# Performance work log

Measured on AMD Instinct MI355X. Metric: run time of the kernel, lower is better.

The kernel has to match this reference:

```python
import jax, jax.numpy as jnp
import numpy as np


def table_operator(A, B):
    # A, B: (size, batch). Returns (16, size, batch) of soft logic-gate outputs.
    AB = A * B
    A_or_B = A + B - AB
    A_xor_B = A + B - 2.0 * AB
    return jnp.stack([
        jnp.zeros_like(A),          # 0: FALSE
        AB,                         # 1: A AND B
        A - AB,                     # 2: A AND NOT B
        A,                          # 3: A
        B - AB,                     # 4: NOT A AND B
        B,                          # 5: B
        A_xor_B,                    # 6: A XOR B
        A_or_B,                     # 7: A OR B
        1.0 - A_or_B,               # 8: NOR
        1.0 - A_xor_B,              # 9: XNOR
        1.0 - B,                    # 10: NOT B
        1.0 - B + AB,               # 11: B -> A
        1.0 - A,                    # 12: NOT A
        1.0 - A + AB,               # 13: A -> B
        1.0 - AB,                   # 14: NAND
        jnp.ones_like(A),           # 15: TRUE
    ], axis=0)


def setup_inputs() -> dict:
    key = jax.random.key(0)
    k1, k2, k3, k4 = jax.random.split(key, 4)
    prev_size, size, batch = 1024, 1024, 16384
    return {
        "prev_layer_output": jax.random.uniform(k1, (prev_size, batch), jnp.float32),
        "input_A_weights": jax.random.normal(k2, (size, prev_size), jnp.float32),
        "input_B_weights": jax.random.normal(k3, (size, prev_size), jnp.float32),
        "table_weights": jax.random.normal(k4, (16, size), jnp.float32),
    }


def reference(prev_layer_output, input_A_weights, input_B_weights, table_weights):
    # Inference path (torch.is_grad_enabled() == False, drop_out_rate == 0):
    # plain softmaxes, no multiplier shift, no dropout. GradFactor is identity in fwd.
    pA = jax.nn.softmax(input_A_weights, axis=1)   # (size, prev_size)
    pB = jax.nn.softmax(input_B_weights, axis=1)
    pT = jax.nn.softmax(table_weights, axis=0)     # (16, size)
    a = pA @ prev_layer_output                     # (size, batch)
    b = pB @ prev_layer_output                     # (size, batch)
    gates = table_operator(a, b)                   # (16, size, batch)
    return jnp.sum(gates * pT[:, :, None], axis=0)  # (size, batch)
```

## Files before the change

kernel.cpp:

```cpp
#include <hip/hip_runtime.h>
#include <hip/hip_bf16.h>


typedef __attribute__((ext_vector_type(8))) short bf16x8;
typedef __attribute__((ext_vector_type(4))) float f32x4;

__device__ __forceinline__ void gload_lds16(const void* g, void* l) {
    __builtin_amdgcn_global_load_lds(
        (const __attribute__((address_space(1))) void*)g,
        (__attribute__((address_space(3))) void*)l, 16, 0, 0);
}

__global__ __launch_bounds__(256) void softmax_rows_bf16(
    const float* __restrict__ WA, const float* __restrict__ WB,
    __hip_bfloat16* __restrict__ PA, __hip_bfloat16* __restrict__ PB,
    int rows, int cols)
{
    const int b = blockIdx.x;
    const float* W;
    __hip_bfloat16* P;
    if (b < rows) { W = WA + (size_t)b * cols;          P = PA + (size_t)b * cols; }
    else          { W = WB + (size_t)(b - rows) * cols; P = PB + (size_t)(b - rows) * cols; }

    const int t = threadIdx.x;
    const int wave = t >> 6, lane = t & 63;

    float4 v = *(const float4*)&W[t * 4];
    float mx = fmaxf(fmaxf(v.x, v.y), fmaxf(v.z, v.w));
    #pragma unroll
    for (int off = 32; off; off >>= 1) mx = fmaxf(mx, __shfl_xor(mx, off));

    __shared__ float redmax[4];
    __shared__ float redsum[4];
    if (lane == 0) redmax[wave] = mx;
    __syncthreads();
    mx = fmaxf(fmaxf(redmax[0], redmax[1]), fmaxf(redmax[2], redmax[3]));

    float e0 = __expf(v.x - mx), e1 = __expf(v.y - mx);
    float e2 = __expf(v.z - mx), e3 = __expf(v.w - mx);
    float s = e0 + e1 + e2 + e3;
    #pragma unroll
    for (int off = 32; off; off >>= 1) s += __shfl_xor(s, off);
    if (lane == 0) redsum[wave] = s;
    __syncthreads();
    s = redsum[0] + redsum[1] + redsum[2] + redsum[3];

    const float inv = 1.0f / s;
    __align__(8) __hip_bfloat16 o[4];
    o[0] = __float2bfloat16(e0 * inv);
    o[1] = __float2bfloat16(e1 * inv);
    o[2] = __float2bfloat16(e2 * inv);
    o[3] = __float2bfloat16(e3 * inv);
    *(uint2*)&P[t * 4] = *(const uint2*)o;
}

__global__ void table_coef(const float* __restrict__ TW, float4* __restrict__ coef, int size)
{
    const int s = blockIdx.x * blockDim.x + threadIdx.x;
    if (s >= size) return;
    float p[16];
    float mx = -1e30f;
    #pragma unroll
    for (int g = 0; g < 16; ++g) { p[g] = TW[g * size + s]; mx = fmaxf(mx, p[g]); }
    float sum = 0.f;
    #pragma unroll
    for (int g = 0; g < 16; ++g) { p[g] = __expf(p[g] - mx); sum += p[g]; }
    const float inv = 1.0f / sum;
    #pragma unroll
    for (int g = 0; g < 16; ++g) p[g] *= inv;

    float w0  = p[8] + p[9] + p[10] + p[11] + p[12] + p[13] + p[14] + p[15];
    float wA  = p[2] + p[3] + p[6] + p[7] - p[8] - p[9] - p[12] - p[13];
    float wB  = p[4] + p[5] + p[6] + p[7] - p[8] - p[9] - p[10] - p[11];
    float wAB = p[1] - p[2] - p[4] - 2.f * p[6] - p[7]
              + p[8] + 2.f * p[9] + p[11] + p[13] - p[14];
    coef[s] = make_float4(w0, wA, wB, wAB);
}

__global__ __launch_bounds__(256) void transpose_bf16(
    const float* __restrict__ prev, __hip_bfloat16* __restrict__ prevT,
    int K, int N)
{
    __shared__ float ls[64][65];
    const int k0 = blockIdx.y * 64, n0 = blockIdx.x * 64;
    const int t = threadIdx.x;

    {
        const int kr = t >> 4, nc = (t & 15) * 4;
        #pragma unroll
        for (int i = 0; i < 4; ++i) {
            const int k = i * 16 + kr;
            float4 v = *(const float4*)&prev[(size_t)(k0 + k) * N + n0 + nc];
            ls[k][nc + 0] = v.x; ls[k][nc + 1] = v.y;
            ls[k][nc + 2] = v.z; ls[k][nc + 3] = v.w;
        }
    }
    __syncthreads();
    {
        const int n = t >> 2, kc = (t & 3) * 16;
        __align__(16) __hip_bfloat16 tmp[16];
        #pragma unroll
        for (int j = 0; j < 16; ++j) tmp[j] = __float2bfloat16(ls[kc + j][n]);
        __hip_bfloat16* dst = &prevT[(size_t)(n0 + n) * K + k0 + kc];
        *(uint4*)(dst + 0) = *(const uint4*)&tmp[0];
        *(uint4*)(dst + 8) = *(const uint4*)&tmp[8];
    }
}

constexpr int Kd = 1024;
constexpr int Nd = 16384;

__global__ __launch_bounds__(512, 2) void dual_gemm8(
    const __hip_bfloat16* __restrict__ pA,
    const __hip_bfloat16* __restrict__ pB,
    const __hip_bfloat16* __restrict__ prevT,
    const float4* __restrict__ coef,
    float* __restrict__ out)
{
    __shared__ __align__(16) char smem[131072];

    const int t_ = threadIdx.x;
    const int wave = t_ >> 6, lane = t_ & 63;
    const int wr = wave >> 2, wc = wave & 3;
    const int m0 = blockIdx.y * 128;
    const int n0 = blockIdx.x * 256;

    const int fr  = lane & 15;
    const int kg  = lane >> 4;
    const int fsw = fr & 7;
    const int c0 = (kg ^ fsw) * 16;
    const int c1 = ((4 + kg) ^ fsw) * 16;
    const int aoffs = (wr * 128 + fr) * 128;
    const int boffs = 32768 + (wc * 64 + fr) * 128;

    const int sr  = lane >> 3;
    const int swz = ((lane & 7) ^ sr) * 8;
    const int r0  = wave * 16 + sr;
    const __hip_bfloat16* gA0 = pA    + (size_t)(m0 + r0) * Kd + swz;
    const __hip_bfloat16* gA1 = pB    + (size_t)(m0 + r0) * Kd + swz;
    const __hip_bfloat16* gB0 = prevT + (size_t)(n0 + r0) * Kd + swz;
    const __hip_bfloat16* gB1 = prevT + (size_t)(n0 + 128 + r0) * Kd + swz;

    f32x4 acc[8][4] = {};
    bf16x8 a[8], b[8];

#define STG(GP, BB, HOFF, KT) {                                             \
    char* lb = smem + (BB) + (HOFF) + wave * 2048;                          \
    gload_lds16((GP) + (KT), lb);                                           \
    gload_lds16((GP) + (KT) + 8 * Kd, lb + 1024); }

#define RD_ALO(BB) _Pragma("unroll") for (int i = 0; i < 4; ++i) {          \
    a[i*2]   = *(const bf16x8*)(smem + (BB) + aoffs + i * 2048 + c0);       \
    a[i*2+1] = *(const bf16x8*)(smem + (BB) + aoffs + i * 2048 + c1); }
#define RD_AHI(BB) _Pragma("unroll") for (int i = 0; i < 4; ++i) {          \
    a[i*2]   = *(const bf16x8*)(smem + (BB) + aoffs + 8192 + i * 2048 + c0);\
    a[i*2+1] = *(const bf16x8*)(smem + (BB) + aoffs + 8192 + i * 2048 + c1); }
#define RD_BLO(BB) _Pragma("unroll") for (int j = 0; j < 2; ++j) {          \
    b[j*2]   = *(const bf16x8*)(smem + (BB) + boffs + j * 2048 + c0);       \
    b[j*2+1] = *(const bf16x8*)(smem + (BB) + boffs + j * 2048 + c1); }
#define RD_BHI(BB) _Pragma("unroll") for (int j = 0; j < 2; ++j) {          \
    b[4+j*2]   = *(const bf16x8*)(smem + (BB) + boffs + 4096 + j * 2048 + c0); \
    b[4+j*2+1] = *(const bf16x8*)(smem + (BB) + boffs + 4096 + j * 2048 + c1); }

#define BAR __builtin_amdgcn_s_barrier()
#define VMW(S) asm volatile("s_waitcnt " S ::: "memory")

#define MM(I0, J0, BB0)                                                     \
    asm volatile("s_waitcnt lgkmcnt(0)" ::: "memory");                      \
    __builtin_amdgcn_sched_barrier(0);                                      \
    __builtin_amdgcn_s_setprio(1);                                          \
    _Pragma("unroll") for (int i = 0; i < 4; ++i)                           \
    _Pragma("unroll") for (int j = 0; j < 2; ++j)                           \
    _Pragma("unroll") for (int ks = 0; ks < 2; ++ks)                        \
        acc[(I0)+i][(J0)+j] = __builtin_amdgcn_mfma_f32_16x16x32_bf16(      \
            a[i*2+ks], b[(BB0)+j*2+ks], acc[(I0)+i][(J0)+j], 0, 0, 0);      \
    __builtin_amdgcn_s_setprio(0);

#define TILE(T, CURB, NXTB, SA, SB, VM1) {                                  \
    RD_ALO(CURB) RD_BLO(CURB)                                               \
    if (SA) STG(gA0, NXTB, 0, ((T)+1)*64)                                   \
    asm volatile("s_waitcnt lgkmcnt(8)" ::: "memory");                      \
    VMW(VM1); BAR;                                                          \
    MM(0, 0, 0) BAR;                                                        \
    RD_BHI(CURB)                                                            \
    if (SA) STG(gA1, NXTB, 16384, ((T)+1)*64)                               \
    VMW("vmcnt(6)"); BAR;                                                   \
    MM(0, 2, 4) BAR;                                                        \
    RD_AHI(CURB)                                                            \
    if (SB) STG(gB0, CURB, 32768, ((T)+2)*64)                               \
    VMW("vmcnt(6)"); BAR;                                                   \
    MM(4, 2, 4) BAR;                                                        \
    if (SB) STG(gB1, CURB, 49152, ((T)+2)*64)                               \
    VMW("vmcnt(6)"); BAR;                                                   \
    MM(4, 0, 0) BAR;                                                        \
}

    STG(gB0, 0, 32768, 0)
    STG(gB1, 0, 49152, 0)
    STG(gA0, 0, 0,     0)
    STG(gA1, 0, 16384, 0)
    STG(gB0, 65536, 32768, 64)
    STG(gB1, 65536, 49152, 64)
    VMW("vmcnt(4)");
    BAR;

    for (int t = 0; t < 14; t += 2) {
        TILE(t,     0,     65536, 1, 1, "vmcnt(6)")
        TILE(t + 1, 65536, 0,     1, 1, "vmcnt(6)")
    }
    TILE(14, 0,     65536, 1, 0, "vmcnt(6)")
    TILE(15, 65536, 0,     0, 0, "vmcnt(0)")

#undef TILE
#undef MM
#undef STG
#undef RD_ALO
#undef RD_AHI
#undef RD_BLO
#undef RD_BHI
#undef BAR
#undef VMW

    __syncthreads();
    if (wr == 1) {
        #pragma unroll
        for (int i = 0; i < 8; ++i) {
            #pragma unroll
            for (int j = 0; j < 4; ++j) {
                const int off = ((((wc * 8 + i) * 4 + j) * 64) + lane) * 16;
                *(f32x4*)(smem + off) = acc[i][j];
            }
        }
    }
    __syncthreads();
    if (wr == 0) {
        const int hi = lane >> 4;
        #pragma unroll
        for (int i = 0; i < 8; ++i) {
            float4 cc[4];
            #pragma unroll
            for (int r = 0; r < 4; ++r) cc[r] = coef[m0 + i * 16 + hi * 4 + r];
            #pragma unroll
            for (int j = 0; j < 4; ++j) {
                const f32x4 bb = *(const f32x4*)(smem + ((((wc * 8 + i) * 4 + j) * 64) + lane) * 16);
                const int n = n0 + wc * 64 + j * 16 + fr;
                #pragma unroll
                for (int r = 0; r < 4; ++r) {
                    const int m = m0 + i * 16 + hi * 4 + r;
                    const float aa = acc[i][j][r];
                    out[(size_t)m * Nd + n] = cc[r].x + cc[r].y * aa + cc[r].z * bb[r]
                                            + cc[r].w * (aa * bb[r]);
                }
            }
        }
    }
}

extern "C" void kernel_launch(void* const* d_in, const int* in_sizes, int n_in,
                              void* d_out, int out_size, void* d_ws, size_t ws_size,
                              hipStream_t stream)
{
    const float* prev = (const float*)d_in[0];
    const float* WA   = (const float*)d_in[1];
    const float* WB   = (const float*)d_in[2];
    const float* TW   = (const float*)d_in[3];
    float* out = (float*)d_out;

    const int size      = in_sizes[3] / 16;
    const int prev_size = in_sizes[1] / size;
    const int batch     = in_sizes[0] / prev_size;

    char* ws = (char*)d_ws;
    __hip_bfloat16* prevT = (__hip_bfloat16*)ws;
    size_t off = (size_t)batch * prev_size * sizeof(__hip_bfloat16);
    __hip_bfloat16* pA = (__hip_bfloat16*)(ws + off);
    off += (size_t)size * prev_size * sizeof(__hip_bfloat16);
    __hip_bfloat16* pB = (__hip_bfloat16*)(ws + off);
    off += (size_t)size * prev_size * sizeof(__hip_bfloat16);
    float4* coef = (float4*)(ws + off);

    softmax_rows_bf16<<<dim3(2 * size), dim3(256), 0, stream>>>(
        WA, WB, pA, pB, size, prev_size);
    table_coef<<<dim3((size + 255) / 256), dim3(256), 0, stream>>>(TW, coef, size);
    transpose_bf16<<<dim3(batch / 64, prev_size / 64), dim3(256), 0, stream>>>(
        prev, prevT, prev_size, batch);
    dual_gemm8<<<dim3(batch / 256, size / 128), dim3(512), 0, stream>>>(
        pA, pB, prevT, coef, out);
}
```

Before: 91.29 us.

## Load A operands directly from global into registers, stage only B in LDS

The main GEMM loop stops staging the pA/pB weight panels through LDS. Each wave now loads its A fragments straight from global memory into registers, with low and high halves loaded separately. Only the prevT tile is double-buffered in LDS, read once per K tile and used for all four column fragments. This cuts LDS traffic and barriers per K step, but exposes global load latency with a blunt vmcnt(0) wait per iteration and raises register pressure from two A fragment sets.

```diff
diff --git a/kernel.cpp b/kernel.cpp
--- a/kernel.cpp
+++ b/kernel.cpp
@@ -128,98 +128,81 @@
     const int fr  = lane & 15;
     const int kg  = lane >> 4;
     const int fsw = fr & 7;
-    const int c0 = (kg ^ fsw) * 16;
-    const int c1 = ((4 + kg) ^ fsw) * 16;
-    const int aoffs = (wr * 128 + fr) * 128;
-    const int boffs = 32768 + (wc * 64 + fr) * 128;
+    const int cc0 = (kg ^ fsw) * 16;
+    const int cc1 = ((4 + kg) ^ fsw) * 16;
+    const int boffs = (wc * 64 + fr) * 128;
 
     const int sr  = lane >> 3;
     const int swz = ((lane & 7) ^ sr) * 8;
     const int r0  = wave * 16 + sr;
-    const __hip_bfloat16* gA0 = pA    + (size_t)(m0 + r0) * Kd + swz;
-    const __hip_bfloat16* gA1 = pB    + (size_t)(m0 + r0) * Kd + swz;
     const __hip_bfloat16* gB0 = prevT + (size_t)(n0 + r0) * Kd + swz;
     const __hip_bfloat16* gB1 = prevT + (size_t)(n0 + 128 + r0) * Kd + swz;
 
+    const __hip_bfloat16* gPan = (wr ? pB : pA) + (size_t)(m0 + fr) * Kd + kg * 8;
+
     f32x4 acc[8][4] = {};
-    bf16x8 a[8], b[8];
-
-#define STG(GP, BB, HOFF, KT) {                                             \
-    char* lb = smem + (BB) + (HOFF) + wave * 2048;                          \
-    gload_lds16((GP) + (KT), lb);                                           \
-    gload_lds16((GP) + (KT) + 8 * Kd, lb + 1024); }
-
-#define RD_ALO(BB) _Pragma("unroll") for (int i = 0; i < 4; ++i) {          \
-    a[i*2]   = *(const bf16x8*)(smem + (BB) + aoffs + i * 2048 + c0);       \
-    a[i*2+1] = *(const bf16x8*)(smem + (BB) + aoffs + i * 2048 + c1); }
-#define RD_AHI(BB) _Pragma("unroll") for (int i = 0; i < 4; ++i) {          \
-    a[i*2]   = *(const bf16x8*)(smem + (BB) + aoffs + 8192 + i * 2048 + c0);\
-    a[i*2+1] = *(const bf16x8*)(smem + (BB) + aoffs + 8192 + i * 2048 + c1); }
-#define RD_BLO(BB) _Pragma("unroll") for (int j = 0; j < 2; ++j) {          \
-    b[j*2]   = *(const bf16x8*)(smem + (BB) + boffs + j * 2048 + c0);       \
-    b[j*2+1] = *(const bf16x8*)(smem + (BB) + boffs + j * 2048 + c1); }
-#define RD_BHI(BB) _Pragma("unroll") for (int j = 0; j < 2; ++j) {          \
-    b[4+j*2]   = *(const bf16x8*)(smem + (BB) + boffs + 4096 + j * 2048 + c0); \
-    b[4+j*2+1] = *(const bf16x8*)(smem + (BB) + boffs + 4096 + j * 2048 + c1); }
-
-#define BAR __builtin_amdgcn_s_barrier()
-#define VMW(S) asm volatile("s_waitcnt " S ::: "memory")
-
-#define MM(I0, J0, BB0)                                                     \
+    bf16x8 aLo[8], aHi[8], b[8];
+
+#define STG_B(T, BB) {                                                      \
+    char* lb = smem + (BB) + wave * 2048;                                   \
+    gload_lds16(gB0 + (T) * 64,           lb);                              \
+    gload_lds16(gB0 + (T) * 64 + 8 * Kd,  lb + 1024);                       \
+    gload_lds16(gB1 + (T) * 64,           lb + 16384);                      \
+    gload_lds16(gB1 + (T) * 64 + 8 * Kd,  lb + 17408);                      \
+    __builtin_amdgcn_sched_barrier(0); }
+
+#define LD_ALO(T) { _Pragma("unroll") for (int i = 0; i < 4; ++i) {         \
+    aLo[i*2]   = *(const bf16x8*)(gPan + (size_t)(i*16) * Kd + (T)*64);     \
+    aLo[i*2+1] = *(const bf16x8*)(gPan + (size_t)(i*16) * Kd + (T)*64 + 32);} \
+    __builtin_amdgcn_sched_barrier(0); }
+
+#define LD_AHI(T) { _Pragma("unroll") for (int i = 0; i < 4; ++i) {         \
+    aHi[i*2]   = *(const bf16x8*)(gPan + (size_t)(64+i*16) * Kd + (T)*64);  \
+    aHi[i*2+1] = *(const bf16x8*)(gPan + (size_t)(64+i*16) * Kd + (T)*64 + 32);} \
+    __builtin_amdgcn_sched_barrier(0); }
+
+#define RD_B8(BB) { _Pragma("unroll") for (int j = 0; j < 4; ++j) {         \
+    b[j*2]   = *(const bf16x8*)(smem + (BB) + boffs + j * 2048 + cc0);      \
+    b[j*2+1] = *(const bf16x8*)(smem + (BB) + boffs + j * 2048 + cc1); } }
+
+#define MM32(AR, I0)                                                        \
     asm volatile("s_waitcnt lgkmcnt(0)" ::: "memory");                      \
     __builtin_amdgcn_sched_barrier(0);                                      \
     __builtin_amdgcn_s_setprio(1);                                          \
     _Pragma("unroll") for (int i = 0; i < 4; ++i)                           \
-    _Pragma("unroll") for (int j = 0; j < 2; ++j)                           \
+    _Pragma("unroll") for (int j = 0; j < 4; ++j)                           \
     _Pragma("unroll") for (int ks = 0; ks < 2; ++ks)                        \
-        acc[(I0)+i][(J0)+j] = __builtin_amdgcn_mfma_f32_16x16x32_bf16(      \
-            a[i*2+ks], b[(BB0)+j*2+ks], acc[(I0)+i][(J0)+j], 0, 0, 0);      \
+        acc[(I0)+i][j] = __builtin_amdgcn_mfma_f32_16x16x32_bf16(           \
+            AR[i*2+ks], b[j*2+ks], acc[(I0)+i][j], 0, 0, 0);                \
     __builtin_amdgcn_s_setprio(0);
 
-#define TILE(T, CURB, NXTB, SA, SB, VM1) {                                  \
-    RD_ALO(CURB) RD_BLO(CURB)                                               \
-    if (SA) STG(gA0, NXTB, 0, ((T)+1)*64)                                   \
-    asm volatile("s_waitcnt lgkmcnt(8)" ::: "memory");                      \
-    VMW(VM1); BAR;                                                          \
-    MM(0, 0, 0) BAR;                                                        \
-    RD_BHI(CURB)                                                            \
-    if (SA) STG(gA1, NXTB, 16384, ((T)+1)*64)                               \
-    VMW("vmcnt(6)"); BAR;                                                   \
-    MM(0, 2, 4) BAR;                                                        \
-    RD_AHI(CURB)                                                            \
-    if (SB) STG(gB0, CURB, 32768, ((T)+2)*64)                               \
-    VMW("vmcnt(6)"); BAR;                                                   \
-    MM(4, 2, 4) BAR;                                                        \
-    if (SB) STG(gB1, CURB, 49152, ((T)+2)*64)                               \
-    VMW("vmcnt(6)"); BAR;                                                   \
-    MM(4, 0, 0) BAR;                                                        \
-}
-
-    STG(gB0, 0, 32768, 0)
-    STG(gB1, 0, 49152, 0)
-    STG(gA0, 0, 0,     0)
-    STG(gA1, 0, 16384, 0)
-    STG(gB0, 65536, 32768, 64)
-    STG(gB1, 65536, 49152, 64)
-    VMW("vmcnt(4)");
-    BAR;
-
-    for (int t = 0; t < 14; t += 2) {
-        TILE(t,     0,     65536, 1, 1, "vmcnt(6)")
-        TILE(t + 1, 65536, 0,     1, 1, "vmcnt(6)")
-    }
-    TILE(14, 0,     65536, 1, 0, "vmcnt(6)")
-    TILE(15, 65536, 0,     0, 0, "vmcnt(0)")
-
-#undef TILE
-#undef MM
-#undef STG
-#undef RD_ALO
-#undef RD_AHI
-#undef RD_BLO
-#undef RD_BHI
-#undef BAR
-#undef VMW
+    STG_B(0, 0)
+    LD_ALO(0)
+    LD_AHI(0)
+
+    for (int t = 0; t < 15; ++t) {
+        const int cb = (t & 1) << 15;
+        const int nb = cb ^ 32768;
+        asm volatile("s_waitcnt vmcnt(0)" ::: "memory");
+        __builtin_amdgcn_s_barrier();
+        RD_B8(cb)
+        STG_B(t + 1, nb)
+        MM32(aLo, 0)
+        LD_ALO(t + 1)
+        MM32(aHi, 4)
+        LD_AHI(t + 1)
+    }
+    asm volatile("s_waitcnt vmcnt(0)" ::: "memory");
+    __builtin_amdgcn_s_barrier();
+    RD_B8(32768)
+    MM32(aLo, 0)
+    MM32(aHi, 4)
+
+#undef MM32
+#undef RD_B8
+#undef LD_ALO
+#undef LD_AHI
+#undef STG_B
 
     __syncthreads();
     if (wr == 1) {
```

Result: slower. 182.5 us (+99.9%).
